# Kernel tuning notes

Measured on AMD Instinct MI355X. Metric: run time of the kernel, lower is better.

Reference implementation:

```python
import jax, jax.numpy as jnp
import numpy as np

V = 32000; D = 1024; H = 16; L = 2; T = 2048; B = 4; C = 32000
DH = D // H
EPS = 1e-5


def layernorm(x, g, b):
    mu = jnp.mean(x, axis=-1, keepdims=True)
    var = jnp.mean((x - mu) ** 2, axis=-1, keepdims=True)
    return (x - mu) * jax.lax.rsqrt(var + EPS) * g + b


def setup_inputs() -> dict:
    key = jax.random.key(0)
    ks = jax.random.split(key, 16)
    s = 0.02
    return {
        "tokens": jax.random.randint(ks[0], (B, T), 0, V),
        "embed_W": jax.random.normal(ks[1], (V, D), jnp.float32) * s,
        "pos_W": jax.random.normal(ks[2], (T, D), jnp.float32) * s,
        "ln_g": jnp.ones((L, D), jnp.float32),
        "ln_b": jnp.zeros((L, D), jnp.float32),
        "qkv_W": jax.random.normal(ks[3], (L, D, 3 * D), jnp.float32) * s,
        "qkv_b": jnp.zeros((L, 3 * D), jnp.float32),
        "out_W": jax.random.normal(ks[4], (L, D, D), jnp.float32) * s,
        "out_b": jnp.zeros((L, D), jnp.float32),
        "lnf_g": jnp.ones((D,), jnp.float32),
        "lnf_b": jnp.zeros((D,), jnp.float32),
        "head_W": jax.random.normal(ks[5], (D, C), jnp.float32) * s,
        "head_b": jnp.zeros((C,), jnp.float32),
    }


def attn_block(x, g, b, Wqkv, bqkv, Wo, bo):
    # pre-LN attention + residual. NOTE: original module defines an MLP but never calls it.
    h = layernorm(x, g, b)
    qkv = h @ Wqkv + bqkv                      # [B,T,3D]
    q, k, v = jnp.split(qkv, 3, axis=-1)
    q = q.reshape(B, T, H, DH)
    k = k.reshape(B, T, H, DH)
    v = v.reshape(B, T, H, DH)
    scores = jnp.einsum("bqhd,bkhd->bhqk", q, k) / np.sqrt(DH)
    causal = jnp.tril(jnp.ones((T, T), bool))
    scores = jnp.where(causal, scores, -jnp.inf)
    attn = jax.nn.softmax(scores, axis=-1)
    o = jnp.einsum("bhqk,bkhd->bqhd", attn, v).reshape(B, T, D)
    return x + o @ Wo + bo


def reference(tokens, embed_W, pos_W, ln_g, ln_b, qkv_W, qkv_b, out_W, out_b,
              lnf_g, lnf_b, head_W, head_b):
    h = embed_W[tokens] + pos_W[jnp.arange(T)][None, :, :]   # [B,T,D]
    for i in range(L):
        h = attn_block(h, ln_g[i], ln_b[i], qkv_W[i], qkv_b[i], out_W[i], out_b[i])
    h = layernorm(h, lnf_g, lnf_b)
    logits = h[:, -1] @ head_W + head_b                      # [B,C]
    return logits
```

## Files before the change

kernel.cpp:

```cpp
#include <hip/hip_runtime.h>

typedef __attribute__((ext_vector_type(8))) __bf16 bf16x8;
typedef __attribute__((ext_vector_type(4))) __bf16 bf16x4;
typedef __attribute__((ext_vector_type(4))) float f32x4;
typedef unsigned long long ull;

static constexpr int kB = 4, kT = 2048, kD = 1024, kH = 16;
static constexpr int kC = 32000, kM = 8192, k3D = 3072, kQK = 2048;

#define MFMA16(a, b, c) __builtin_amdgcn_mfma_f32_16x16x32_bf16((a), (b), (c), 0, 0, 0)

__device__ __forceinline__ void gload_lds16(const __bf16* g, __bf16* l) {
  __builtin_amdgcn_global_load_lds(
      (const __attribute__((address_space(1))) unsigned int*)(const void*)g,
      (__attribute__((address_space(3))) unsigned int*)(void*)l, 16, 0, 0);
}

__global__ __launch_bounds__(256) void embed_kernel(const int* __restrict__ tok,
                                                    const float* __restrict__ embW,
                                                    const float* __restrict__ posW,
                                                    float* __restrict__ h) {
  const int row = blockIdx.x;
  const int t = row & (kT - 1);
  const int tk = tok[row];
  const f32x4 e = ((const f32x4*)(embW + (size_t)tk * kD))[threadIdx.x];
  const f32x4 p = ((const f32x4*)(posW + (size_t)t * kD))[threadIdx.x];
  ((f32x4*)(h + (size_t)row * kD))[threadIdx.x] = e + p;
}

template <bool BF16OUT>
__global__ __launch_bounds__(256) void ln_kernel(const float* __restrict__ x,
                                                 const float* __restrict__ g,
                                                 const float* __restrict__ bb,
                                                 void* __restrict__ outp) {
  const int row = blockIdx.x, tid = threadIdx.x;
  const f32x4 xv = ((const f32x4*)(x + (size_t)row * kD))[tid];
  float s  = xv[0] + xv[1] + xv[2] + xv[3];
  float s2 = xv[0]*xv[0] + xv[1]*xv[1] + xv[2]*xv[2] + xv[3]*xv[3];
  #pragma unroll
  for (int off = 1; off < 64; off <<= 1) {
    s  += __shfl_xor(s, off);
    s2 += __shfl_xor(s2, off);
  }
  __shared__ float red[8];
  const int w = tid >> 6;
  if ((tid & 63) == 0) { red[w*2] = s; red[w*2+1] = s2; }
  __syncthreads();
  s  = red[0] + red[2] + red[4] + red[6];
  s2 = red[1] + red[3] + red[5] + red[7];
  const float mu  = s * (1.f / kD);
  const float var = s2 * (1.f / kD) - mu * mu;
  const float rs  = rsqrtf(var + 1e-5f);
  const f32x4 gv = ((const f32x4*)g)[tid];
  const f32x4 bv = ((const f32x4*)bb)[tid];
  if constexpr (BF16OUT) {
    bf16x4 o;
    #pragma unroll
    for (int i = 0; i < 4; i++) o[i] = (__bf16)((xv[i] - mu) * rs * gv[i] + bv[i]);
    ((bf16x4*)((__bf16*)outp + (size_t)row * kD))[tid] = o;
  } else {
    f32x4 o;
    #pragma unroll
    for (int i = 0; i < 4; i++) o[i] = (xv[i] - mu) * rs * gv[i] + bv[i];
    ((f32x4*)((float*)outp + (size_t)row * kD))[tid] = o;
  }
}

__global__ __launch_bounds__(256) void transpose_w_kernel(const float* __restrict__ W,
                                                          __bf16* __restrict__ WT,
                                                          int K, int N) {
  __shared__ float sh[32][33];
  const int tx = threadIdx.x & 31, ty = threadIdx.x >> 5;
  const int ntile = N >> 5;
  const int c0 = (blockIdx.x % ntile) << 5;
  const int r0 = (blockIdx.x / ntile) << 5;
  #pragma unroll
  for (int i = 0; i < 4; i++) {
    const int r = ty + i * 8;
    sh[r][tx] = W[(size_t)(r0 + r) * N + c0 + tx];
  }
  __syncthreads();
  #pragma unroll
  for (int i = 0; i < 4; i++) {
    const int cc = ty + i * 8;
    WT[(size_t)(c0 + cc) * K + r0 + tx] = (__bf16)sh[tx][cc];
  }
}

template <bool OUT_BF16>
__global__ __launch_bounds__(256) void gemm_bt_kernel(const __bf16* __restrict__ A,
                                                      const __bf16* __restrict__ BT,
                                                      const float* __restrict__ bias,
                                                      const float* resid,
                                                      float* outf,
                                                      __bf16* outb,
                                                      __bf16* vtp,
                                                      int N, int K, int ldc, int vt_c0,
                                                      int bm_mult, int bm_add) {
  __shared__ __bf16 As[128 * 64];
  __shared__ __bf16 Bs[128 * 64];
  const int tid = threadIdx.x;
  const int lane = tid & 63, w = tid >> 6;
  int wg = (int)blockIdx.x;
  const int nwg = gridDim.x;
  wg = (wg & 7) * (nwg >> 3) + (wg >> 3);
  const int nbn = N >> 7;
  const int bm = (wg / nbn) * bm_mult + bm_add;
  const int bn = wg % nbn;
  const int wr = (w >> 1) * 64, wc = (w & 1) * 64;
  const int lrow = lane & 15, lk8 = (lane >> 4) * 8;

  const int srow = lane >> 3;
  const int scol = (lane & 7) * 8;
  const __bf16* gA = A + (size_t)(bm * 128) * K;
  const __bf16* gB = BT + (size_t)(bn * 128) * K;

  f32x4 acc[4][4] = {};

  for (int k0 = 0; k0 < K; k0 += 64) {
    __syncthreads();
    #pragma unroll
    for (int i = 0; i < 4; i++) {
      const int c = w * 4 + i;
      const int row = c * 8 + srow;
      gload_lds16(gA + (size_t)row * K + k0 + scol, As + c * 512);
      gload_lds16(gB + (size_t)row * K + k0 + scol, Bs + c * 512);
    }
    __syncthreads();
    #pragma unroll
    for (int ks = 0; ks < 2; ks++) {
      bf16x8 af[4], bf[4];
      #pragma unroll
      for (int mt = 0; mt < 4; mt++)
        af[mt] = *(const bf16x8*)(As + (wr + mt * 16 + lrow) * 64 + ks * 32 + lk8);
      #pragma unroll
      for (int nt = 0; nt < 4; nt++)
        bf[nt] = *(const bf16x8*)(Bs + (wc + nt * 16 + lrow) * 64 + ks * 32 + lk8);
      #pragma unroll
      for (int mt = 0; mt < 4; mt++)
        #pragma unroll
        for (int nt = 0; nt < 4; nt++)
          acc[mt][nt] = MFMA16(af[mt], bf[nt], acc[mt][nt]);
    }
  }

  #pragma unroll
  for (int mt = 0; mt < 4; mt++) {
    const int row0 = bm * 128 + wr + mt * 16 + (lane >> 4) * 4;
    #pragma unroll
    for (int nt = 0; nt < 4; nt++) {
      const int col = bn * 128 + wc + nt * 16 + lrow;
      const float bsv = bias[col];
      if (vtp && col >= vt_c0) {
        const int vd = col - vt_c0;
        const int bb_ = row0 >> 11, t = row0 & (kT - 1);
        bf16x4 pk;
        #pragma unroll
        for (int r = 0; r < 4; r++) pk[r] = (__bf16)(acc[mt][nt][r] + bsv);
        *(bf16x4*)(vtp + ((size_t)((bb_ << 4) + (vd >> 6)) * 64 + (vd & 63)) * kT + t) = pk;
      } else {
        #pragma unroll
        for (int r = 0; r < 4; r++) {
          const size_t idx = (size_t)(row0 + r) * ldc + col;
          const float v = acc[mt][nt][r] + bsv;
          if constexpr (OUT_BF16) {
            outb[idx] = (__bf16)v;
          } else {
            outf[idx] = v + resid[idx];
          }
        }
      }
    }
  }
}

template <int MODE>
__global__ __launch_bounds__(256) void flash_kernel(const __bf16* __restrict__ qkv,
                                                    const __bf16* __restrict__ vtg,
                                                    __bf16* __restrict__ o,
                                                    float* __restrict__ part_acc,
                                                    float* __restrict__ part_ml,
                                                    int nsub) {
  constexpr float SC = 0.18033688011112042f;
  __shared__ __bf16 Qs[64 * 64];
  __shared__ __bf16 Ks[64 * 64];
  __shared__ __bf16 Vs[64 * 64];
  const int tid = threadIdx.x, lane = tid & 63, w = tid >> 6;
  int wg = (int)blockIdx.x;
  const int nwg = gridDim.x;
  wg = (wg & 7) * (nwg >> 3) + (wg >> 3);
  const int sub = wg % nsub, bh = wg / nsub;
  const int b = bh >> 4, hh = bh & 15;
  const int g = lane >> 4, qown = lane & 15;
  const int sslot = (lane & 7) ^ ((lane >> 3) & 7);
  const int swz = (qown & 7) << 3;
  const size_t row0 = (size_t)b * kT;
  const int NS = (MODE == 0) ? 2 : 1;

  for (int s = 0; s < NS; s++) {
    int qt, ktlo, kthi;
    if constexpr (MODE == 0) {
      qt = s ? (2 * nsub - 1 - sub) : sub;
      ktlo = 0; kthi = qt + 1;
    } else {
      qt = 31; ktlo = sub * 4; kthi = ktlo + 4;
    }

    __syncthreads();
    #pragma unroll
    for (int j = 0; j < 2; j++) {
      const int r = w * 16 + j * 8 + (lane >> 3);
      gload_lds16(qkv + (row0 + qt * 64 + r) * kQK + hh * 64 + sslot * 8,
                  Qs + (w * 16 + j * 8) * 64);
    }
    __syncthreads();
    bf16x8 qf[2];
    #pragma unroll
    for (int ks = 0; ks < 2; ks++) {
      bf16x8 qr = *(const bf16x8*)(Qs + (w * 16 + qown) * 64 + ((ks * 32 + 8 * g) ^ swz));
      #pragma unroll
      for (int i = 0; i < 8; i++) qf[ks][i] = (__bf16)((float)qr[i] * SC);
    }

    float m_run = -1e30f, l_run = 0.f;
    f32x4 acc[4] = {};

    for (int kt = ktlo; kt < kthi; kt++) {
      __syncthreads();
      #pragma unroll
      for (int j = 0; j < 2; j++) {
        const int r = w * 16 + j * 8 + (lane >> 3);
        gload_lds16(qkv + (row0 + kt * 64 + r) * kQK + 1024 + hh * 64 + sslot * 8,
                    Ks + (w * 16 + j * 8) * 64);
        gload_lds16(vtg + ((size_t)bh * 64 + r) * kT + kt * 64 + sslot * 8,
                    Vs + (w * 16 + j * 8) * 64);
      }
      __syncthreads();

      f32x4 sv[4] = {};
      #pragma unroll
      for (int nt = 0; nt < 4; nt++) {
        const int kr = nt * 16 + qown;
        #pragma unroll
        for (int ks = 0; ks < 2; ks++) {
          bf16x8 kf = *(const bf16x8*)(Ks + kr * 64 + ((ks * 32 + 8 * g) ^ swz));
          sv[nt] = MFMA16(kf, qf[ks], sv[nt]);
        }
      }
      if (kt == qt) {
        #pragma unroll
        for (int nt = 0; nt < 4; nt++)
          #pragma unroll
          for (int r = 0; r < 4; r++)
            if (nt * 16 + 4 * g + r > w * 16 + qown) sv[nt][r] = -1e30f;
      }

      float mx = -1e30f;
      #pragma unroll
      for (int nt = 0; nt < 4; nt++)
        #pragma unroll
        for (int r = 0; r < 4; r++) mx = fmaxf(mx, sv[nt][r]);
      mx = fmaxf(mx, __shfl_xor(mx, 16));
      mx = fmaxf(mx, __shfl_xor(mx, 32));
      const float mnew = fmaxf(m_run, mx);
      const float fsc = exp2f(m_run - mnew);
      m_run = mnew;
      float ps = 0.f;
      ull quad[4];
      #pragma unroll
      for (int nt = 0; nt < 4; nt++) {
        union { bf16x4 v; ull u; } qd;
        #pragma unroll
        for (int r = 0; r < 4; r++) {
          const float p = exp2f(sv[nt][r] - mnew);
          ps += p;
          qd.v[r] = (__bf16)p;
        }
        quad[nt] = qd.u;
      }
      ps += __shfl_xor(ps, 16);
      ps += __shfl_xor(ps, 32);
      l_run = l_run * fsc + ps;

      float fr[4];
      #pragma unroll
      for (int r = 0; r < 4; r++) fr[r] = __shfl(fsc, 20 * g + r);
      #pragma unroll
      for (int nt = 0; nt < 4; nt++)
        #pragma unroll
        for (int r = 0; r < 4; r++) acc[nt][r] *= fr[r];

      bf16x8 pf[2];
      #pragma unroll
      for (int ks = 0; ks < 2; ks++) {
        const int src = (g & 1) * 32 + qown;
        const ull t0 = __shfl(quad[2 * ks],     src);
        const ull t1 = __shfl(quad[2 * ks + 1], src);
        const ull lo = (g & 2) ? t1 : t0;
        const ull t2 = __shfl(quad[2 * ks],     src + 16);
        const ull t3 = __shfl(quad[2 * ks + 1], src + 16);
        const ull hi = (g & 2) ? t3 : t2;
        union { ull u[2]; bf16x8 v; } pk;
        pk.u[0] = lo; pk.u[1] = hi;
        pf[ks] = pk.v;
      }

      #pragma unroll
      for (int nt = 0; nt < 4; nt++) {
        const int vr = nt * 16 + qown;
        #pragma unroll
        for (int ks = 0; ks < 2; ks++) {
          bf16x8 vf = *(const bf16x8*)(Vs + vr * 64 + ((ks * 32 + 8 * g) ^ swz));
          acc[nt] = MFMA16(pf[ks], vf, acc[nt]);
        }
      }
    }

    if constexpr (MODE == 0) {
      const float li = 1.f / l_run;
      float lr[4];
      #pragma unroll
      for (int r = 0; r < 4; r++) lr[r] = __shfl(li, 20 * g + r);
      #pragma unroll
      for (int r = 0; r < 4; r++) {
        const int t = qt * 64 + w * 16 + 4 * g + r;
        #pragma unroll
        for (int nt = 0; nt < 4; nt++)
          o[(row0 + t) * kD + hh * 64 + nt * 16 + qown] = (__bf16)(acc[nt][r] * lr[r]);
      }
    } else {
      const int tile = bh * nsub + sub;
      #pragma unroll
      for (int r = 0; r < 4; r++) {
        const int rr = w * 16 + 4 * g + r;
        #pragma unroll
        for (int nt = 0; nt < 4; nt++)
          part_acc[(size_t)tile * 4096 + rr * 64 + nt * 16 + qown] = acc[nt][r];
      }
      if (g == 0) {
        part_ml[tile * 128 + w * 16 + qown] = m_run;
        part_ml[tile * 128 + 64 + w * 16 + qown] = l_run;
      }
    }
  }
}

__global__ __launch_bounds__(256) void flash_merge_kernel(const float* __restrict__ part_acc,
                                                          const float* __restrict__ part_ml,
                                                          __bf16* __restrict__ o) {
  const int bh = blockIdx.x, b = bh >> 4, hh = bh & 15;
  for (int e = threadIdx.x; e < 4096; e += 256) {
    const int row = e >> 6, d = e & 63;
    float mstar = -1e30f;
    #pragma unroll
    for (int kc = 0; kc < 8; kc++)
      mstar = fmaxf(mstar, part_ml[(bh * 8 + kc) * 128 + row]);
    float lstar = 0.f, osum = 0.f;
    #pragma unroll
    for (int kc = 0; kc < 8; kc++) {
      const float wgt = exp2f(part_ml[(bh * 8 + kc) * 128 + row] - mstar);
      lstar += wgt * part_ml[(bh * 8 + kc) * 128 + 64 + row];
      osum  += wgt * part_acc[(size_t)(bh * 8 + kc) * 4096 + e];
    }
    o[(size_t)(b * kT + 1984 + row) * kD + hh * 64 + d] = (__bf16)(osum / lstar);
  }
}

__global__ __launch_bounds__(256) void proj_last_kernel(const __bf16* __restrict__ o,
                                                        const float* __restrict__ W,
                                                        const float* __restrict__ bias,
                                                        const float* __restrict__ h,
                                                        float* __restrict__ out4) {
  const int b = blockIdx.y;
  const int j = blockIdx.x * 256 + threadIdx.x;
  __shared__ float ov[kD];
  const __bf16* orow = o + (size_t)(b * kT + kT - 1) * kD;
  for (int i = threadIdx.x; i < kD; i += 256) ov[i] = (float)orow[i];
  __syncthreads();
  float acc = 0.f;
  #pragma unroll 8
  for (int k = 0; k < kD; k++) acc = fmaf(ov[k], W[(size_t)k * kD + j], acc);
  out4[b * kD + j] = h[(size_t)(b * kT + kT - 1) * kD + j] + bias[j] + acc;
}

__global__ __launch_bounds__(256) void head_kernel(const float* __restrict__ hl,
                                                   const float* __restrict__ W,
                                                   const float* __restrict__ hb,
                                                   float* __restrict__ out) {
  const int j = blockIdx.x * 256 + threadIdx.x;
  __shared__ float sh[kB * kD];
  for (int i = threadIdx.x; i < kB * kD; i += 256) sh[i] = hl[i];
  __syncthreads();
  float a0 = 0.f, a1 = 0.f, a2 = 0.f, a3 = 0.f;
  #pragma unroll 8
  for (int k = 0; k < kD; k++) {
    const float wv = W[(size_t)k * kC + j];
    a0 = fmaf(sh[k], wv, a0);
    a1 = fmaf(sh[kD + k], wv, a1);
    a2 = fmaf(sh[2 * kD + k], wv, a2);
    a3 = fmaf(sh[3 * kD + k], wv, a3);
  }
  const float bb = hb[j];
  out[j] = a0 + bb;
  out[kC + j] = a1 + bb;
  out[2 * kC + j] = a2 + bb;
  out[3 * kC + j] = a3 + bb;
}

extern "C" void kernel_launch(void* const* d_in, const int* in_sizes, int n_in,
                              void* d_out, int out_size, void* d_ws, size_t ws_size,
                              hipStream_t stream) {
  const int*   tokens = (const int*)d_in[0];
  const float* embW   = (const float*)d_in[1];
  const float* posW   = (const float*)d_in[2];
  const float* ln_g   = (const float*)d_in[3];
  const float* ln_b   = (const float*)d_in[4];
  const float* qkv_W  = (const float*)d_in[5];
  const float* qkv_b  = (const float*)d_in[6];
  const float* out_W  = (const float*)d_in[7];
  const float* out_b  = (const float*)d_in[8];
  const float* lnf_g  = (const float*)d_in[9];
  const float* lnf_b  = (const float*)d_in[10];
  const float* headW  = (const float*)d_in[11];
  const float* headb  = (const float*)d_in[12];
  float* logits = (float*)d_out;

  char* ws = (char*)d_ws;
  float*  h     = (float*)(ws);
  __bf16* hn    = (__bf16*)(ws + 33554432);
  __bf16* qkv   = (__bf16*)(ws + 50331648);
  __bf16* Vt    = (__bf16*)(ws + 83886080);
  __bf16* ob    = (__bf16*)(ws + 100663296);
  __bf16* WqkvT = (__bf16*)(ws + 117440512);
  __bf16* WoT   = (__bf16*)(ws + 130613248);
  float*  hl4   = (float*)(ws + 132710400);
  float*  hl    = (float*)(ws + 132726784);
  float* part_acc = (float*)(ws + 33554432);
  float* part_ml  = (float*)(ws + 33554432 + 8388608);

  transpose_w_kernel<<<(kD/32)*(k3D/32), 256, 0, stream>>>(qkv_W, WqkvT, kD, k3D);
  transpose_w_kernel<<<(kD/32)*(k3D/32), 256, 0, stream>>>(qkv_W + (size_t)kD*k3D,
                                                           WqkvT + (size_t)k3D*kD, kD, k3D);
  transpose_w_kernel<<<(kD/32)*(kD/32), 256, 0, stream>>>(out_W, WoT, kD, kD);

  embed_kernel<<<kM, 256, 0, stream>>>(tokens, embW, posW, h);

  ln_kernel<true><<<kM, 256, 0, stream>>>(h, ln_g, ln_b, hn);
  gemm_bt_kernel<true><<<(kM/128)*(k3D/128), 256, 0, stream>>>(
      hn, WqkvT, qkv_b, nullptr, nullptr, qkv, Vt, k3D, kD, kQK, 2048, 1, 0);
  flash_kernel<0><<<kB*kH*16, 256, 0, stream>>>(qkv, Vt, ob, nullptr, nullptr, 16);
  gemm_bt_kernel<false><<<(kM/128)*(kD/128), 256, 0, stream>>>(
      ob, WoT, out_b, h, h, nullptr, nullptr, kD, kD, kD, 1 << 30, 1, 0);

  ln_kernel<true><<<kM, 256, 0, stream>>>(h, ln_g + kD, ln_b + kD, hn);
  gemm_bt_kernel<true><<<(kM/128)*(2048/128), 256, 0, stream>>>(
      hn, WqkvT + (size_t)k3D*kD + (size_t)kD*kD, qkv_b + k3D + kD,
      nullptr, nullptr, qkv + 1024, Vt, 2048, kD, kQK, 1024, 1, 0);
  gemm_bt_kernel<true><<<kB*(kD/128), 256, 0, stream>>>(
      hn, WqkvT + (size_t)k3D*kD, qkv_b + k3D,
      nullptr, nullptr, qkv, nullptr, kD, kD, kQK, 1 << 30, 16, 15);
  flash_kernel<1><<<kB*kH*8, 256, 0, stream>>>(qkv, Vt, nullptr, part_acc, part_ml, 8);
  flash_merge_kernel<<<kB*kH, 256, 0, stream>>>(part_acc, part_ml, ob);
  proj_last_kernel<<<dim3(kD/256, kB), 256, 0, stream>>>(ob, out_W + (size_t)kD*kD,
                                                         out_b + kD, h, hl4);

  ln_kernel<false><<<kB, 256, 0, stream>>>(hl4, lnf_g, lnf_b, hl);
  head_kernel<<<kC/256, 256, 0, stream>>>(hl, headW, headb, logits);
}
```

Baseline: 535.1 us.

## Double-buffer flash K/V, fuse embed+LN, merge transposes, split-K head

Several independent changes land together. The flash kernel now double-buffers its K/V tiles in LDS, prefetching the next tile while computing the current one. It also skips the online-softmax rescale when the running max has not grown by more than a threshold, and raises wave priority around the MFMA blocks, as the GEMM does too. The embedding is fused with the first layernorm, the three weight-transpose launches become one kernel, and the head GEMV splits K across four waves with more blocks to raise parallelism. The costs are more LDS use in flash, a lazy-rescale path whose numerics depend on the threshold, and extra shared-memory reductions in the head kernel.

```diff
diff --git a/kernel.cpp b/kernel.cpp
--- a/kernel.cpp
+++ b/kernel.cpp
@@ -16,16 +16,42 @@
       (__attribute__((address_space(3))) unsigned int*)(void*)l, 16, 0, 0);
 }
 
-__global__ __launch_bounds__(256) void embed_kernel(const int* __restrict__ tok,
-                                                    const float* __restrict__ embW,
-                                                    const float* __restrict__ posW,
-                                                    float* __restrict__ h) {
-  const int row = blockIdx.x;
+__global__ __launch_bounds__(256) void embed_ln_kernel(const int* __restrict__ tok,
+                                                       const float* __restrict__ embW,
+                                                       const float* __restrict__ posW,
+                                                       const float* __restrict__ g,
+                                                       const float* __restrict__ bb,
+                                                       float* __restrict__ h,
+                                                       __bf16* __restrict__ hn) {
+  const int row = blockIdx.x, tid = threadIdx.x;
   const int t = row & (kT - 1);
   const int tk = tok[row];
-  const f32x4 e = ((const f32x4*)(embW + (size_t)tk * kD))[threadIdx.x];
-  const f32x4 p = ((const f32x4*)(posW + (size_t)t * kD))[threadIdx.x];
-  ((f32x4*)(h + (size_t)row * kD))[threadIdx.x] = e + p;
+  const f32x4 e = ((const f32x4*)(embW + (size_t)tk * kD))[tid];
+  const f32x4 p = ((const f32x4*)(posW + (size_t)t * kD))[tid];
+  const f32x4 xv = e + p;
+  ((f32x4*)(h + (size_t)row * kD))[tid] = xv;
+  float s  = xv[0] + xv[1] + xv[2] + xv[3];
+  float s2 = xv[0]*xv[0] + xv[1]*xv[1] + xv[2]*xv[2] + xv[3]*xv[3];
+  #pragma unroll
+  for (int off = 1; off < 64; off <<= 1) {
+    s  += __shfl_xor(s, off);
+    s2 += __shfl_xor(s2, off);
+  }
+  __shared__ float red[8];
+  const int w = tid >> 6;
+  if ((tid & 63) == 0) { red[w*2] = s; red[w*2+1] = s2; }
+  __syncthreads();
+  s  = red[0] + red[2] + red[4] + red[6];
+  s2 = red[1] + red[3] + red[5] + red[7];
+  const float mu  = s * (1.f / kD);
+  const float var = s2 * (1.f / kD) - mu * mu;
+  const float rs  = rsqrtf(var + 1e-5f);
+  const f32x4 gv = ((const f32x4*)g)[tid];
+  const f32x4 bv = ((const f32x4*)bb)[tid];
+  bf16x4 o;
+  #pragma unroll
+  for (int i = 0; i < 4; i++) o[i] = (__bf16)((xv[i] - mu) * rs * gv[i] + bv[i]);
+  ((bf16x4*)(hn + (size_t)row * kD))[tid] = o;
 }
 
 template <bool BF16OUT>
@@ -66,14 +92,20 @@
   }
 }
 
-__global__ __launch_bounds__(256) void transpose_w_kernel(const float* __restrict__ W,
-                                                          __bf16* __restrict__ WT,
-                                                          int K, int N) {
+__global__ __launch_bounds__(256) void transpose_all_kernel(const float* __restrict__ qkv_W,
+                                                            const float* __restrict__ out_W,
+                                                            __bf16* __restrict__ WqkvT,
+                                                            __bf16* __restrict__ WoT) {
   __shared__ float sh[32][33];
+  const int bid = blockIdx.x;
+  const float* W; __bf16* WT; int N, tile;
+  if (bid < 3072)      { W = qkv_W;                   WT = WqkvT;                    N = k3D; tile = bid; }
+  else if (bid < 6144) { W = qkv_W + (size_t)kD*k3D;  WT = WqkvT + (size_t)k3D*kD;   N = k3D; tile = bid - 3072; }
+  else                 { W = out_W;                   WT = WoT;                      N = kD;  tile = bid - 6144; }
   const int tx = threadIdx.x & 31, ty = threadIdx.x >> 5;
   const int ntile = N >> 5;
-  const int c0 = (blockIdx.x % ntile) << 5;
-  const int r0 = (blockIdx.x / ntile) << 5;
+  const int c0 = (tile % ntile) << 5;
+  const int r0 = (tile / ntile) << 5;
   #pragma unroll
   for (int i = 0; i < 4; i++) {
     const int r = ty + i * 8;
@@ -83,7 +115,7 @@
   #pragma unroll
   for (int i = 0; i < 4; i++) {
     const int cc = ty + i * 8;
-    WT[(size_t)(c0 + cc) * K + r0 + tx] = (__bf16)sh[tx][cc];
+    WT[(size_t)(c0 + cc) * kD + r0 + tx] = (__bf16)sh[tx][cc];
   }
 }
 
@@ -136,11 +168,13 @@
       #pragma unroll
       for (int nt = 0; nt < 4; nt++)
         bf[nt] = *(const bf16x8*)(Bs + (wc + nt * 16 + lrow) * 64 + ks * 32 + lk8);
+      __builtin_amdgcn_s_setprio(1);
       #pragma unroll
       for (int mt = 0; mt < 4; mt++)
         #pragma unroll
         for (int nt = 0; nt < 4; nt++)
           acc[mt][nt] = MFMA16(af[mt], bf[nt], acc[mt][nt]);
+      __builtin_amdgcn_s_setprio(0);
     }
   }
 
@@ -183,8 +217,8 @@
                                                     int nsub) {
   constexpr float SC = 0.18033688011112042f;
   __shared__ __bf16 Qs[64 * 64];
-  __shared__ __bf16 Ks[64 * 64];
-  __shared__ __bf16 Vs[64 * 64];
+  __shared__ __bf16 Ks[2][64 * 64];
+  __shared__ __bf16 Vs[2][64 * 64];
   const int tid = threadIdx.x, lane = tid & 63, w = tid >> 6;
   int wg = (int)blockIdx.x;
   const int nwg = gridDim.x;
@@ -196,6 +230,7 @@
   const int swz = (qown & 7) << 3;
   const size_t row0 = (size_t)b * kT;
   const int NS = (MODE == 0) ? 2 : 1;
+  const int r8 = lane >> 3;
 
   for (int s = 0; s < NS; s++) {
     int qt, ktlo, kthi;
@@ -209,9 +244,13 @@
     __syncthreads();
     #pragma unroll
     for (int j = 0; j < 2; j++) {
-      const int r = w * 16 + j * 8 + (lane >> 3);
+      const int r = w * 16 + j * 8 + r8;
       gload_lds16(qkv + (row0 + qt * 64 + r) * kQK + hh * 64 + sslot * 8,
                   Qs + (w * 16 + j * 8) * 64);
+      gload_lds16(qkv + (row0 + ktlo * 64 + r) * kQK + 1024 + hh * 64 + sslot * 8,
+                  Ks[0] + (w * 16 + j * 8) * 64);
+      gload_lds16(vtg + ((size_t)bh * 64 + r) * kT + ktlo * 64 + sslot * 8,
+                  Vs[0] + (w * 16 + j * 8) * 64);
     }
     __syncthreads();
     bf16x8 qf[2];
@@ -224,29 +263,32 @@
 
     float m_run = -1e30f, l_run = 0.f;
     f32x4 acc[4] = {};
+    int cur = 0;
 
     for (int kt = ktlo; kt < kthi; kt++) {
-      __syncthreads();
-      #pragma unroll
-      for (int j = 0; j < 2; j++) {
-        const int r = w * 16 + j * 8 + (lane >> 3);
-        gload_lds16(qkv + (row0 + kt * 64 + r) * kQK + 1024 + hh * 64 + sslot * 8,
-                    Ks + (w * 16 + j * 8) * 64);
-        gload_lds16(vtg + ((size_t)bh * 64 + r) * kT + kt * 64 + sslot * 8,
-                    Vs + (w * 16 + j * 8) * 64);
-      }
-      __syncthreads();
+      if (kt + 1 < kthi) {
+        #pragma unroll
+        for (int j = 0; j < 2; j++) {
+          const int r = w * 16 + j * 8 + r8;
+          gload_lds16(qkv + (row0 + (kt + 1) * 64 + r) * kQK + 1024 + hh * 64 + sslot * 8,
+                      Ks[cur ^ 1] + (w * 16 + j * 8) * 64);
+          gload_lds16(vtg + ((size_t)bh * 64 + r) * kT + (kt + 1) * 64 + sslot * 8,
+                      Vs[cur ^ 1] + (w * 16 + j * 8) * 64);
+        }
+      }
 
       f32x4 sv[4] = {};
+      __builtin_amdgcn_s_setprio(1);
       #pragma unroll
       for (int nt = 0; nt < 4; nt++) {
         const int kr = nt * 16 + qown;
         #pragma unroll
         for (int ks = 0; ks < 2; ks++) {
-          bf16x8 kf = *(const bf16x8*)(Ks + kr * 64 + ((ks * 32 + 8 * g) ^ swz));
+          bf16x8 kf = *(const bf16x8*)(Ks[cur] + kr * 64 + ((ks * 32 + 8 * g) ^ swz));
           sv[nt] = MFMA16(kf, qf[ks], sv[nt]);
         }
       }
+      __builtin_amdgcn_s_setprio(0);
       if (kt == qt) {
         #pragma unroll
         for (int nt = 0; nt < 4; nt++)
@@ -262,33 +304,50 @@
         for (int r = 0; r < 4; r++) mx = fmaxf(mx, sv[nt][r]);
       mx = fmaxf(mx, __shfl_xor(mx, 16));
       mx = fmaxf(mx, __shfl_xor(mx, 32));
-      const float mnew = fmaxf(m_run, mx);
-      const float fsc = exp2f(m_run - mnew);
-      m_run = mnew;
+
       float ps = 0.f;
       ull quad[4];
-      #pragma unroll
-      for (int nt = 0; nt < 4; nt++) {
-        union { bf16x4 v; ull u; } qd;
-        #pragma unroll
-        for (int r = 0; r < 4; r++) {
-          const float p = exp2f(sv[nt][r] - mnew);
-          ps += p;
-          qd.v[r] = (__bf16)p;
+      if (__all(mx - m_run <= 8.0f)) {
+        #pragma unroll
+        for (int nt = 0; nt < 4; nt++) {
+          union { bf16x4 v; ull u; } qd;
+          #pragma unroll
+          for (int r = 0; r < 4; r++) {
+            const float p = exp2f(sv[nt][r] - m_run);
+            ps += p;
+            qd.v[r] = (__bf16)p;
+          }
+          quad[nt] = qd.u;
         }
-        quad[nt] = qd.u;
-      }
-      ps += __shfl_xor(ps, 16);
-      ps += __shfl_xor(ps, 32);
-      l_run = l_run * fsc + ps;
-
-      float fr[4];
-      #pragma unroll
-      for (int r = 0; r < 4; r++) fr[r] = __shfl(fsc, 20 * g + r);
-      #pragma unroll
-      for (int nt = 0; nt < 4; nt++)
-        #pragma unroll
-        for (int r = 0; r < 4; r++) acc[nt][r] *= fr[r];
+        ps += __shfl_xor(ps, 16);
+        ps += __shfl_xor(ps, 32);
+        l_run += ps;
+      } else {
+        const float mnew = fmaxf(m_run, mx);
+        const float fsc = exp2f(m_run - mnew);
+        m_run = mnew;
+        #pragma unroll
+        for (int nt = 0; nt < 4; nt++) {
+          union { bf16x4 v; ull u; } qd;
+          #pragma unroll
+          for (int r = 0; r < 4; r++) {
+            const float p = exp2f(sv[nt][r] - mnew);
+            ps += p;
+            qd.v[r] = (__bf16)p;
+          }
+          quad[nt] = qd.u;
+        }
+        ps += __shfl_xor(ps, 16);
+        ps += __shfl_xor(ps, 32);
+        l_run = l_run * fsc + ps;
+        float fr[4];
+        #pragma unroll
+        for (int r = 0; r < 4; r++) fr[r] = __shfl(fsc, 20 * g + r);
+        #pragma unroll
+        for (int nt = 0; nt < 4; nt++)
+          #pragma unroll
+          for (int r = 0; r < 4; r++) acc[nt][r] *= fr[r];
+      }
 
       bf16x8 pf[2];
       #pragma unroll
@@ -305,15 +364,20 @@
         pf[ks] = pk.v;
       }
 
+      __builtin_amdgcn_s_setprio(1);
       #pragma unroll
       for (int nt = 0; nt < 4; nt++) {
         const int vr = nt * 16 + qown;
         #pragma unroll
         for (int ks = 0; ks < 2; ks++) {
-          bf16x8 vf = *(const bf16x8*)(Vs + vr * 64 + ((ks * 32 + 8 * g) ^ swz));
+          bf16x8 vf = *(const bf16x8*)(Vs[cur] + vr * 64 + ((ks * 32 + 8 * g) ^ swz));
           acc[nt] = MFMA16(pf[ks], vf, acc[nt]);
         }
       }
+      __builtin_amdgcn_s_setprio(0);
+
+      __syncthreads();
+      cur ^= 1;
     }
 
     if constexpr (MODE == 0) {
@@ -387,24 +451,29 @@
                                                    const float* __restrict__ W,
                                                    const float* __restrict__ hb,
                                                    float* __restrict__ out) {
-  const int j = blockIdx.x * 256 + threadIdx.x;
+  const int jj = threadIdx.x & 63, ks = threadIdx.x >> 6;
+  const int j = blockIdx.x * 64 + jj;
   __shared__ float sh[kB * kD];
+  __shared__ float red[4][kB][64];
   for (int i = threadIdx.x; i < kB * kD; i += 256) sh[i] = hl[i];
   __syncthreads();
-  float a0 = 0.f, a1 = 0.f, a2 = 0.f, a3 = 0.f;
-  #pragma unroll 8
-  for (int k = 0; k < kD; k++) {
+  float a[kB] = {};
+  const int k0 = ks * 256;
+  #pragma unroll 4
+  for (int k = k0; k < k0 + 256; k++) {
     const float wv = W[(size_t)k * kC + j];
-    a0 = fmaf(sh[k], wv, a0);
-    a1 = fmaf(sh[kD + k], wv, a1);
-    a2 = fmaf(sh[2 * kD + k], wv, a2);
-    a3 = fmaf(sh[3 * kD + k], wv, a3);
-  }
-  const float bb = hb[j];
-  out[j] = a0 + bb;
-  out[kC + j] = a1 + bb;
-  out[2 * kC + j] = a2 + bb;
-  out[3 * kC + j] = a3 + bb;
+    #pragma unroll
+    for (int bb = 0; bb < kB; bb++) a[bb] = fmaf(sh[bb * kD + k], wv, a[bb]);
+  }
+  #pragma unroll
+  for (int bb = 0; bb < kB; bb++) red[ks][bb][jj] = a[bb];
+  __syncthreads();
+  if (ks == 0) {
+    const float bv = hb[j];
+    #pragma unroll
+    for (int bb = 0; bb < kB; bb++)
+      out[(size_t)bb * kC + j] = red[0][bb][jj] + red[1][bb][jj] + red[2][bb][jj] + red[3][bb][jj] + bv;
+  }
 }
 
 extern "C" void kernel_launch(void* const* d_in, const int* in_sizes, int n_in,
@@ -438,14 +507,9 @@
   float* part_acc = (float*)(ws + 33554432);
   float* part_ml  = (float*)(ws + 33554432 + 8388608);
 
-  transpose_w_kernel<<<(kD/32)*(k3D/32), 256, 0, stream>>>(qkv_W, WqkvT, kD, k3D);
-  transpose_w_kernel<<<(kD/32)*(k3D/32), 256, 0, stream>>>(qkv_W + (size_t)kD*k3D,
-                                                           WqkvT + (size_t)k3D*kD, kD, k3D);
-  transpose_w_kernel<<<(kD/32)*(kD/32), 256, 0, stream>>>(out_W, WoT, kD, kD);
-
-  embed_kernel<<<kM, 256, 0, stream>>>(tokens, embW, posW, h);
-
-  ln_kernel<true><<<kM, 256, 0, stream>>>(h, ln_g, ln_b, hn);
+  transpose_all_kernel<<<7168, 256, 0, stream>>>(qkv_W, out_W, WqkvT, WoT);
+  embed_ln_kernel<<<kM, 256, 0, stream>>>(tokens, embW, posW, ln_g, ln_b, h, hn);
+
   gemm_bt_kernel<true><<<(kM/128)*(k3D/128), 256, 0, stream>>>(
       hn, WqkvT, qkv_b, nullptr, nullptr, qkv, Vt, k3D, kD, kQK, 2048, 1, 0);
   flash_kernel<0><<<kB*kH*16, 256, 0, stream>>>(qkv, Vt, ob, nullptr, nullptr, 16);
@@ -465,5 +529,5 @@
                                                          out_b + kD, h, hl4);
 
   ln_kernel<false><<<kB, 256, 0, stream>>>(hl4, lnf_g, lnf_b, hl);
-  head_kernel<<<kC/256, 256, 0, stream>>>(hl, headW, headb, logits);
-}
+  head_kernel<<<500, 256, 0, stream>>>(hl, headW, headb, logits);
+}
```

Measured after the change: 480.8 us. -10.1%, faster.
